# Optimization experiments

Hardware: AMD Instinct MI355X
Metric: run time of the kernel (lower is better)

Reference implementation:

```python
import jax, jax.numpy as jnp
import numpy as np

INPUT_SIZE = 32
HIDDEN = 64


def _lstm_layer(x, W_ih, W_hh, b_ih, b_hh):
    """Single LSTM layer, batch_first x: (B, T, D) -> (B, T, H).
    PyTorch gate order: i, f, g, o."""
    B, T, _ = x.shape
    H = W_hh.shape[1]
    # Precompute input contribution for all timesteps (the big GEMM).
    xg = jnp.einsum('btd,gd->btg', x, W_ih) + b_ih + b_hh  # (B, T, 4H)
    xg = jnp.swapaxes(xg, 0, 1)  # (T, B, 4H) for scan over time

    def step(carry, g_t):
        h, c = carry
        gates = g_t + h @ W_hh.T  # (B, 4H)
        i, f, g, o = jnp.split(gates, 4, axis=-1)
        c = jax.nn.sigmoid(f) * c + jax.nn.sigmoid(i) * jnp.tanh(g)
        h = jax.nn.sigmoid(o) * jnp.tanh(c)
        return (h, c), h

    h0 = jnp.zeros((B, H), dtype=x.dtype)
    c0 = jnp.zeros((B, H), dtype=x.dtype)
    (_, _), hs = jax.lax.scan(step, (h0, c0), xg)
    return jnp.swapaxes(hs, 0, 1)  # (B, T, H)


def setup_inputs() -> dict:
    key = jax.random.key(0)
    ks = jax.random.split(key, 11)
    B, T, D, H = 1024, 512, INPUT_SIZE, HIDDEN
    s_ih0 = 1.0 / np.sqrt(H)
    u = lambda k, shape: jax.random.uniform(k, shape, jnp.float32, -s_ih0, s_ih0)
    return {
        'x': jax.random.normal(ks[0], (B, T, D), jnp.float32),
        'W_ih0': u(ks[1], (4 * H, D)),
        'W_hh0': u(ks[2], (4 * H, H)),
        'b_ih0': u(ks[3], (4 * H,)),
        'b_hh0': u(ks[4], (4 * H,)),
        'W_ih1': u(ks[5], (4 * H, H)),
        'W_hh1': u(ks[6], (4 * H, H)),
        'b_ih1': u(ks[7], (4 * H,)),
        'b_hh1': u(ks[8], (4 * H,)),
        'W_fc': u(ks[9], (1, H)),
        'b_fc': u(ks[10], (1,)),
    }


def reference(x, W_ih0, W_hh0, b_ih0, b_hh0, W_ih1, W_hh1, b_ih1, b_hh1, W_fc, b_fc):
    h1 = _lstm_layer(x, W_ih0, W_hh0, b_ih0, b_hh0)   # (B, T, H)
    h2 = _lstm_layer(h1, W_ih1, W_hh1, b_ih1, b_hh1)  # (B, T, H)
    last = h2[:, -1, :]                                # (B, H)
    return last @ W_fc.T + b_fc                        # (B, 1)
```

## Files before the change

kernel.cpp:

```cpp
#include <hip/hip_runtime.h>

#define T_STEPS 512

typedef __attribute__((ext_vector_type(8))) short s16x8;
typedef __attribute__((ext_vector_type(4))) float f32x4;

__device__ __forceinline__ short f2bf(float v) {
    unsigned u = __float_as_uint(v);
    return (short)((u + 0x7FFFu + ((u >> 16) & 1u)) >> 16);
}
__device__ __forceinline__ float bf2f(short b) {
    return __uint_as_float(((unsigned)(unsigned short)b) << 16);
}
__device__ __forceinline__ float sigf(float x)  { return 1.f / (1.f + __expf(-x)); }
__device__ __forceinline__ float tanhf_(float x){ float e = __expf(2.f * x); return 1.f - 2.f / (e + 1.f); }

__global__ __launch_bounds__(1024, 4)
void lstm2_mfma(const float* __restrict__ x,
                const float* __restrict__ Wih0, const float* __restrict__ Whh0,
                const float* __restrict__ bih0, const float* __restrict__ bhh0,
                const float* __restrict__ Wih1, const float* __restrict__ Whh1,
                const float* __restrict__ bih1, const float* __restrict__ bhh1,
                const float* __restrict__ Wfc,  const float* __restrict__ bfc,
                float* __restrict__ out)
{
    __shared__ __align__(16) short vinB[2][16][104];
    __shared__ __align__(16) short u1B [2][16][136];
    __shared__ __align__(16) float gbuf0[256 * 4];
    __shared__ __align__(16) float gbuf1[256 * 4];

    const int tid  = threadIdx.x;
    const int w    = tid >> 6;
    const int lane = tid & 63;
    const int n16  = lane & 15;
    const int q4   = lane >> 4;
    const int b0   = blockIdx.x * 4;

    const int rowW = (n16 & 3) * 64 + 4 * w + (n16 >> 2);
    s16x8 a0, a1, a2;
    s16x8 e0, e1, e2, e3;
#pragma unroll
    for (int j = 0; j < 8; ++j) {
        a0[j] = f2bf(Wih0[rowW * 32 + q4 * 8 + j]);
        a1[j] = f2bf(Whh0[rowW * 64 + q4 * 8 + j]);
        a2[j] = f2bf(Whh0[rowW * 64 + 32 + q4 * 8 + j]);
        e0[j] = f2bf(Wih1[rowW * 64 + q4 * 8 + j]);
        e1[j] = f2bf(Wih1[rowW * 64 + 32 + q4 * 8 + j]);
        e2[j] = f2bf(Whh1[rowW * 64 + q4 * 8 + j]);
        e3[j] = f2bf(Whh1[rowW * 64 + 32 + q4 * 8 + j]);
    }

    const int jL = 4 * w + q4;
    f32x4 bias0, bias1;
#pragma unroll
    for (int p_ = 0; p_ < 4; ++p_) {
        bias0[p_] = bih0[p_ * 64 + jL] + bhh0[p_ * 64 + jL];
        bias1[p_] = bih1[p_ * 64 + jL] + bhh1[p_ * 64 + jL];
    }

    const int gwi = jL * 4 + n16;
    const int cw  = w & 3;
    const int cs  = 16 * cw + (lane >> 2);
    const int cb  = lane & 3;
    const int gri = 64 * cw + lane;

    const int nB  = (n16 < 4) ? n16 : 3;

    const bool isx = (w >= 8) && (w < 12) && (n16 >= 4) && (n16 < 12);
    const int  xb  = (w - 8) & 3;
    const int  xk  = q4 * 8 + ((n16 - 4) & 7);
    const float* xp = x + ((size_t)(b0 + xb) * T_STEPS) * 32 + xk;

    for (int i = tid; i < 2 * 16 * 104 / 2; i += 1024) ((int*)vinB)[i] = 0;
    for (int i = tid; i < 2 * 16 * 136 / 2; i += 1024) ((int*)u1B)[i]  = 0;
    __syncthreads();
    if (isx) vinB[0][xb][xk] = f2bf(xp[0]);
    __syncthreads();

    float cst0 = 0.f, cst1 = 0.f;

    for (int it = 0; it <= T_STEPS; ++it) {
        const int p = it & 1;

        float xpre = 0.f;
        const bool havex = isx && (it + 1 < T_STEPS);
        if (havex) xpre = xp[(size_t)(it + 1) * 32];

        const short* vb = &vinB[p][nB][q4 * 8];
        s16x8 vb0 = *(const s16x8*)(vb);
        s16x8 vb1 = *(const s16x8*)(vb + 32);
        s16x8 vb2 = *(const s16x8*)(vb + 64);
        const short* ub = &u1B[p][nB][q4 * 8];
        s16x8 ub0 = *(const s16x8*)(ub);
        s16x8 ub1 = *(const s16x8*)(ub + 32);
        s16x8 ub2 = *(const s16x8*)(ub + 64);
        s16x8 ub3 = *(const s16x8*)(ub + 96);

        f32x4 d0 = __builtin_amdgcn_mfma_f32_16x16x32_bf16(a0, vb0, bias0, 0, 0, 0);
        d0 = __builtin_amdgcn_mfma_f32_16x16x32_bf16(a1, vb1, d0, 0, 0, 0);
        d0 = __builtin_amdgcn_mfma_f32_16x16x32_bf16(a2, vb2, d0, 0, 0, 0);
        f32x4 d1 = __builtin_amdgcn_mfma_f32_16x16x32_bf16(e0, ub0, bias1, 0, 0, 0);
        d1 = __builtin_amdgcn_mfma_f32_16x16x32_bf16(e1, ub1, d1, 0, 0, 0);
        d1 = __builtin_amdgcn_mfma_f32_16x16x32_bf16(e2, ub2, d1, 0, 0, 0);
        d1 = __builtin_amdgcn_mfma_f32_16x16x32_bf16(e3, ub3, d1, 0, 0, 0);

        if (n16 < 4) {
            *(f32x4*)&gbuf0[gwi * 4] = d0;
            *(f32x4*)&gbuf1[gwi * 4] = d1;
        }
        __syncthreads();

        if (w < 4) {
            if (it < T_STEPS) {
                f32x4 g = *(const f32x4*)&gbuf0[gri * 4];
                float cc = sigf(g[1]) * cst0 + sigf(g[0]) * tanhf_(g[2]);
                cst0 = cc;
                short hb = f2bf(sigf(g[3]) * tanhf_(cc));
                vinB[p ^ 1][cb][32 + cs] = hb;
                u1B [p ^ 1][cb][cs]      = hb;
            }
        } else if (w < 8) {
            if (it >= 1) {
                f32x4 g = *(const f32x4*)&gbuf1[gri * 4];
                float cc = sigf(g[1]) * cst1 + sigf(g[0]) * tanhf_(g[2]);
                cst1 = cc;
                u1B[p ^ 1][cb][64 + cs] = f2bf(sigf(g[3]) * tanhf_(cc));
            }
        }
        if (havex) vinB[p ^ 1][xb][xk] = f2bf(xpre);
        __syncthreads();
    }

    if (tid < 4) {
        float s = bfc[0];
#pragma unroll
        for (int k = 0; k < 64; ++k)
            s += bf2f(u1B[1][tid][64 + k]) * Wfc[k];
        out[b0 + tid] = s;
    }
}

extern "C" void kernel_launch(void* const* d_in, const int* in_sizes, int n_in,
                              void* d_out, int out_size, void* d_ws, size_t ws_size,
                              hipStream_t stream) {
    const float* x    = (const float*)d_in[0];
    const float* Wih0 = (const float*)d_in[1];
    const float* Whh0 = (const float*)d_in[2];
    const float* bih0 = (const float*)d_in[3];
    const float* bhh0 = (const float*)d_in[4];
    const float* Wih1 = (const float*)d_in[5];
    const float* Whh1 = (const float*)d_in[6];
    const float* bih1 = (const float*)d_in[7];
    const float* bhh1 = (const float*)d_in[8];
    const float* Wfc  = (const float*)d_in[9];
    const float* bfc  = (const float*)d_in[10];
    float* out = (float*)d_out;

    const int B = out_size;
    dim3 grid(B / 4), block(1024);
    hipLaunchKernelGGL(lstm2_mfma, grid, block, 0, stream,
                       x, Wih0, Whh0, bih0, bhh0,
                       Wih1, Whh1, bih1, bhh1, Wfc, bfc, out);
}
```

Baseline: 584.6 us.

## Halve batch per block to 2 and give each wave two MFMA gate tiles

Each block now handles 2 batch rows with 512 threads instead of 4 rows with 1024. Each wave holds two sets of weight fragments and issues two interleaved independent MFMA chains. The goal is twice as many blocks across the GPU, cheaper block-wide barriers, and more MFMA instruction-level parallelism per wave. In exchange, only 2 of the 16 MFMA columns carry useful batch data, so more MFMA work is wasted per batch row, and register pressure rises.

```diff
diff --git a/kernel.cpp b/kernel.cpp
--- a/kernel.cpp
+++ b/kernel.cpp
@@ -15,7 +15,7 @@
 __device__ __forceinline__ float sigf(float x)  { return 1.f / (1.f + __expf(-x)); }
 __device__ __forceinline__ float tanhf_(float x){ float e = __expf(2.f * x); return 1.f - 2.f / (e + 1.f); }
 
-__global__ __launch_bounds__(1024, 4)
+__global__ __launch_bounds__(512, 4)
 void lstm2_mfma(const float* __restrict__ x,
                 const float* __restrict__ Wih0, const float* __restrict__ Whh0,
                 const float* __restrict__ bih0, const float* __restrict__ bhh0,
@@ -24,55 +24,58 @@
                 const float* __restrict__ Wfc,  const float* __restrict__ bfc,
                 float* __restrict__ out)
 {
-    __shared__ __align__(16) short vinB[2][16][104];
-    __shared__ __align__(16) short u1B [2][16][136];
-    __shared__ __align__(16) float gbuf0[256 * 4];
-    __shared__ __align__(16) float gbuf1[256 * 4];
+    __shared__ __align__(16) short vinB[2][2][104];
+    __shared__ __align__(16) short u1B [2][2][136];
+    __shared__ __align__(16) float gbuf0[128 * 4];
+    __shared__ __align__(16) float gbuf1[128 * 4];
 
     const int tid  = threadIdx.x;
     const int w    = tid >> 6;
     const int lane = tid & 63;
     const int n16  = lane & 15;
     const int q4   = lane >> 4;
-    const int b0   = blockIdx.x * 4;
+    const int b0   = blockIdx.x * 2;
 
-    const int rowW = (n16 & 3) * 64 + 4 * w + (n16 >> 2);
-    s16x8 a0, a1, a2;
-    s16x8 e0, e1, e2, e3;
+    s16x8 a0[2], a1[2], a2[2];
+    s16x8 e0[2], e1[2], e2[2], e3[2];
+    f32x4 bias0[2], bias1[2];
 #pragma unroll
-    for (int j = 0; j < 8; ++j) {
-        a0[j] = f2bf(Wih0[rowW * 32 + q4 * 8 + j]);
-        a1[j] = f2bf(Whh0[rowW * 64 + q4 * 8 + j]);
-        a2[j] = f2bf(Whh0[rowW * 64 + 32 + q4 * 8 + j]);
-        e0[j] = f2bf(Wih1[rowW * 64 + q4 * 8 + j]);
-        e1[j] = f2bf(Wih1[rowW * 64 + 32 + q4 * 8 + j]);
-        e2[j] = f2bf(Whh1[rowW * 64 + q4 * 8 + j]);
-        e3[j] = f2bf(Whh1[rowW * 64 + 32 + q4 * 8 + j]);
+    for (int t = 0; t < 2; ++t) {
+        const int rowW = (n16 & 3) * 64 + 8 * w + 4 * t + (n16 >> 2);
+#pragma unroll
+        for (int j = 0; j < 8; ++j) {
+            a0[t][j] = f2bf(Wih0[rowW * 32 + q4 * 8 + j]);
+            a1[t][j] = f2bf(Whh0[rowW * 64 + q4 * 8 + j]);
+            a2[t][j] = f2bf(Whh0[rowW * 64 + 32 + q4 * 8 + j]);
+            e0[t][j] = f2bf(Wih1[rowW * 64 + q4 * 8 + j]);
+            e1[t][j] = f2bf(Wih1[rowW * 64 + 32 + q4 * 8 + j]);
+            e2[t][j] = f2bf(Whh1[rowW * 64 + q4 * 8 + j]);
+            e3[t][j] = f2bf(Whh1[rowW * 64 + 32 + q4 * 8 + j]);
+        }
+        const int jl = 8 * w + 4 * t + q4;
+#pragma unroll
+        for (int p_ = 0; p_ < 4; ++p_) {
+            bias0[t][p_] = bih0[p_ * 64 + jl] + bhh0[p_ * 64 + jl];
+            bias1[t][p_] = bih1[p_ * 64 + jl] + bhh1[p_ * 64 + jl];
+        }
     }
 
-    const int jL = 4 * w + q4;
-    f32x4 bias0, bias1;
-#pragma unroll
-    for (int p_ = 0; p_ < 4; ++p_) {
-        bias0[p_] = bih0[p_ * 64 + jL] + bhh0[p_ * 64 + jL];
-        bias1[p_] = bih1[p_ * 64 + jL] + bhh1[p_ * 64 + jL];
-    }
+    const int gw0 = ((8 * w + q4) * 2 + n16) * 4;
+    const int gw1 = ((8 * w + 4 + q4) * 2 + n16) * 4;
+    const int cw2 = w & 1;
+    const int cs  = 32 * cw2 + (lane >> 1);
+    const int cb  = lane & 1;
+    const int gri = 64 * cw2 + lane;
 
-    const int gwi = jL * 4 + n16;
-    const int cw  = w & 3;
-    const int cs  = 16 * cw + (lane >> 2);
-    const int cb  = lane & 3;
-    const int gri = 64 * cw + lane;
+    const int nB  = (n16 < 2) ? n16 : 1;
 
-    const int nB  = (n16 < 4) ? n16 : 3;
-
-    const bool isx = (w >= 8) && (w < 12) && (n16 >= 4) && (n16 < 12);
-    const int  xb  = (w - 8) & 3;
-    const int  xk  = q4 * 8 + ((n16 - 4) & 7);
+    const bool isx = (w == 4);
+    const int  xb  = lane >> 5;
+    const int  xk  = lane & 31;
     const float* xp = x + ((size_t)(b0 + xb) * T_STEPS) * 32 + xk;
 
-    for (int i = tid; i < 2 * 16 * 104 / 2; i += 1024) ((int*)vinB)[i] = 0;
-    for (int i = tid; i < 2 * 16 * 136 / 2; i += 1024) ((int*)u1B)[i]  = 0;
+    for (int i = tid; i < 2 * 2 * 104 / 2; i += 512) ((int*)vinB)[i] = 0;
+    for (int i = tid; i < 2 * 2 * 136 / 2; i += 512) ((int*)u1B)[i]  = 0;
     __syncthreads();
     if (isx) vinB[0][xb][xk] = f2bf(xp[0]);
     __syncthreads();
@@ -90,27 +93,38 @@
         s16x8 vb0 = *(const s16x8*)(vb);
         s16x8 vb1 = *(const s16x8*)(vb + 32);
         s16x8 vb2 = *(const s16x8*)(vb + 64);
+
+        f32x4 d0a = __builtin_amdgcn_mfma_f32_16x16x32_bf16(a0[0], vb0, bias0[0], 0, 0, 0);
+        f32x4 d0b = __builtin_amdgcn_mfma_f32_16x16x32_bf16(a0[1], vb0, bias0[1], 0, 0, 0);
+        d0a = __builtin_amdgcn_mfma_f32_16x16x32_bf16(a1[0], vb1, d0a, 0, 0, 0);
+        d0b = __builtin_amdgcn_mfma_f32_16x16x32_bf16(a1[1], vb1, d0b, 0, 0, 0);
+        d0a = __builtin_amdgcn_mfma_f32_16x16x32_bf16(a2[0], vb2, d0a, 0, 0, 0);
+        d0b = __builtin_amdgcn_mfma_f32_16x16x32_bf16(a2[1], vb2, d0b, 0, 0, 0);
+
         const short* ub = &u1B[p][nB][q4 * 8];
         s16x8 ub0 = *(const s16x8*)(ub);
         s16x8 ub1 = *(const s16x8*)(ub + 32);
         s16x8 ub2 = *(const s16x8*)(ub + 64);
         s16x8 ub3 = *(const s16x8*)(ub + 96);
 
-        f32x4 d0 = __builtin_amdgcn_mfma_f32_16x16x32_bf16(a0, vb0, bias0, 0, 0, 0);
-        d0 = __builtin_amdgcn_mfma_f32_16x16x32_bf16(a1, vb1, d0, 0, 0, 0);
-        d0 = __builtin_amdgcn_mfma_f32_16x16x32_bf16(a2, vb2, d0, 0, 0, 0);
-        f32x4 d1 = __builtin_amdgcn_mfma_f32_16x16x32_bf16(e0, ub0, bias1, 0, 0, 0);
-        d1 = __builtin_amdgcn_mfma_f32_16x16x32_bf16(e1, ub1, d1, 0, 0, 0);
-        d1 = __builtin_amdgcn_mfma_f32_16x16x32_bf16(e2, ub2, d1, 0, 0, 0);
-        d1 = __builtin_amdgcn_mfma_f32_16x16x32_bf16(e3, ub3, d1, 0, 0, 0);
+        f32x4 d1a = __builtin_amdgcn_mfma_f32_16x16x32_bf16(e0[0], ub0, bias1[0], 0, 0, 0);
+        f32x4 d1b = __builtin_amdgcn_mfma_f32_16x16x32_bf16(e0[1], ub0, bias1[1], 0, 0, 0);
+        d1a = __builtin_amdgcn_mfma_f32_16x16x32_bf16(e1[0], ub1, d1a, 0, 0, 0);
+        d1b = __builtin_amdgcn_mfma_f32_16x16x32_bf16(e1[1], ub1, d1b, 0, 0, 0);
+        d1a = __builtin_amdgcn_mfma_f32_16x16x32_bf16(e2[0], ub2, d1a, 0, 0, 0);
+        d1b = __builtin_amdgcn_mfma_f32_16x16x32_bf16(e2[1], ub2, d1b, 0, 0, 0);
+        d1a = __builtin_amdgcn_mfma_f32_16x16x32_bf16(e3[0], ub3, d1a, 0, 0, 0);
+        d1b = __builtin_amdgcn_mfma_f32_16x16x32_bf16(e3[1], ub3, d1b, 0, 0, 0);
 
-        if (n16 < 4) {
-            *(f32x4*)&gbuf0[gwi * 4] = d0;
-            *(f32x4*)&gbuf1[gwi * 4] = d1;
+        if (n16 < 2) {
+            *(f32x4*)&gbuf0[gw0] = d0a;
+            *(f32x4*)&gbuf0[gw1] = d0b;
+            *(f32x4*)&gbuf1[gw0] = d1a;
+            *(f32x4*)&gbuf1[gw1] = d1b;
         }
         __syncthreads();
 
-        if (w < 4) {
+        if (w < 2) {
             if (it < T_STEPS) {
                 f32x4 g = *(const f32x4*)&gbuf0[gri * 4];
                 float cc = sigf(g[1]) * cst0 + sigf(g[0]) * tanhf_(g[2]);
@@ -119,7 +133,7 @@
                 vinB[p ^ 1][cb][32 + cs] = hb;
                 u1B [p ^ 1][cb][cs]      = hb;
             }
-        } else if (w < 8) {
+        } else if (w < 4) {
             if (it >= 1) {
                 f32x4 g = *(const f32x4*)&gbuf1[gri * 4];
                 float cc = sigf(g[1]) * cst1 + sigf(g[0]) * tanhf_(g[2]);
@@ -131,7 +145,7 @@
         __syncthreads();
     }
 
-    if (tid < 4) {
+    if (tid < 2) {
         float s = bfc[0];
 #pragma unroll
         for (int k = 0; k < 64; ++k)
@@ -157,7 +171,7 @@
     float* out = (float*)d_out;
 
     const int B = out_size;
-    dim3 grid(B / 4), block(1024);
+    dim3 grid(B / 2), block(512);
     hipLaunchKernelGGL(lstm2_mfma, grid, block, 0, stream,
                        x, Wih0, Whh0, bih0, bhh0,
                        Wih1, Whh1, bih1, bhh1, Wfc, bfc, out);
```

Result: slower. 653.4 us (+11.8%).

## Merge LSTM layer input buffers into one shared LDS buffer and use fast exp/rcp

Applied to the files above, without the earlier changes.

Merges the two per-layer B-operand LDS buffers into one contiguous buffer [x | h1 | h2], so the layer-1 h value is written once and shared by both MFMA chains. This drops one LDS store per step and two B-fragment loads per step. The sigmoid and tanh helpers now call the hardware exp2 and rcp builtins instead of expf and division, and the launch bounds become an explicit waves-per-eu attribute. The single cell-state register works because each wave handles only one layer. The approximate reciprocal adds a small precision loss.

```diff
diff --git a/kernel.cpp b/kernel.cpp
--- a/kernel.cpp
+++ b/kernel.cpp
@@ -12,10 +12,13 @@
 __device__ __forceinline__ float bf2f(short b) {
     return __uint_as_float(((unsigned)(unsigned short)b) << 16);
 }
-__device__ __forceinline__ float sigf(float x)  { return 1.f / (1.f + __expf(-x)); }
-__device__ __forceinline__ float tanhf_(float x){ float e = __expf(2.f * x); return 1.f - 2.f / (e + 1.f); }
+#define LOG2E 1.4426950408889634f
+__device__ __forceinline__ float rcpf(float x)  { return __builtin_amdgcn_rcpf(x); }
+__device__ __forceinline__ float ex2f(float x)  { return __builtin_amdgcn_exp2f(x); }
+__device__ __forceinline__ float sigf(float x)  { return rcpf(1.f + ex2f(-LOG2E * x)); }
+__device__ __forceinline__ float tanhf_(float x){ return 1.f - 2.f * rcpf(ex2f(2.f * LOG2E * x) + 1.f); }
 
-__global__ __launch_bounds__(1024, 4)
+__global__ __launch_bounds__(1024) __attribute__((amdgpu_waves_per_eu(4, 4)))
 void lstm2_mfma(const float* __restrict__ x,
                 const float* __restrict__ Wih0, const float* __restrict__ Whh0,
                 const float* __restrict__ bih0, const float* __restrict__ bhh0,
@@ -24,8 +27,7 @@
                 const float* __restrict__ Wfc,  const float* __restrict__ bfc,
                 float* __restrict__ out)
 {
-    __shared__ __align__(16) short vinB[2][16][104];
-    __shared__ __align__(16) short u1B [2][16][136];
+    __shared__ __align__(16) short bB[2][4][176];
     __shared__ __align__(16) float gbuf0[256 * 4];
     __shared__ __align__(16) float gbuf1[256 * 4];
 
@@ -58,7 +60,7 @@
         bias1[p_] = bih1[p_ * 64 + jL] + bhh1[p_ * 64 + jL];
     }
 
-    const int gwi = jL * 4 + n16;
+    const int gwi = (jL * 4 + n16) * 4;
     const int cw  = w & 3;
     const int cs  = 16 * cw + (lane >> 2);
     const int cb  = lane & 3;
@@ -71,13 +73,12 @@
     const int  xk  = q4 * 8 + ((n16 - 4) & 7);
     const float* xp = x + ((size_t)(b0 + xb) * T_STEPS) * 32 + xk;
 
-    for (int i = tid; i < 2 * 16 * 104 / 2; i += 1024) ((int*)vinB)[i] = 0;
-    for (int i = tid; i < 2 * 16 * 136 / 2; i += 1024) ((int*)u1B)[i]  = 0;
+    for (int i = tid; i < 2 * 4 * 176 / 2; i += 1024) ((int*)bB)[i] = 0;
     __syncthreads();
-    if (isx) vinB[0][xb][xk] = f2bf(xp[0]);
+    if (isx) bB[0][xb][xk] = f2bf(xp[0]);
     __syncthreads();
 
-    float cst0 = 0.f, cst1 = 0.f;
+    float cst = 0.f;
 
     for (int it = 0; it <= T_STEPS; ++it) {
         const int p = it & 1;
@@ -86,48 +87,43 @@
         const bool havex = isx && (it + 1 < T_STEPS);
         if (havex) xpre = xp[(size_t)(it + 1) * 32];
 
-        const short* vb = &vinB[p][nB][q4 * 8];
-        s16x8 vb0 = *(const s16x8*)(vb);
-        s16x8 vb1 = *(const s16x8*)(vb + 32);
-        s16x8 vb2 = *(const s16x8*)(vb + 64);
-        const short* ub = &u1B[p][nB][q4 * 8];
-        s16x8 ub0 = *(const s16x8*)(ub);
-        s16x8 ub1 = *(const s16x8*)(ub + 32);
-        s16x8 ub2 = *(const s16x8*)(ub + 64);
-        s16x8 ub3 = *(const s16x8*)(ub + 96);
+        const short* bp = &bB[p][nB][q4 * 8];
+        s16x8 t0 = *(const s16x8*)(bp);
+        s16x8 t1 = *(const s16x8*)(bp + 32);
+        s16x8 t2 = *(const s16x8*)(bp + 64);
+        s16x8 t3 = *(const s16x8*)(bp + 96);
+        s16x8 t4 = *(const s16x8*)(bp + 128);
 
-        f32x4 d0 = __builtin_amdgcn_mfma_f32_16x16x32_bf16(a0, vb0, bias0, 0, 0, 0);
-        d0 = __builtin_amdgcn_mfma_f32_16x16x32_bf16(a1, vb1, d0, 0, 0, 0);
-        d0 = __builtin_amdgcn_mfma_f32_16x16x32_bf16(a2, vb2, d0, 0, 0, 0);
-        f32x4 d1 = __builtin_amdgcn_mfma_f32_16x16x32_bf16(e0, ub0, bias1, 0, 0, 0);
-        d1 = __builtin_amdgcn_mfma_f32_16x16x32_bf16(e1, ub1, d1, 0, 0, 0);
-        d1 = __builtin_amdgcn_mfma_f32_16x16x32_bf16(e2, ub2, d1, 0, 0, 0);
-        d1 = __builtin_amdgcn_mfma_f32_16x16x32_bf16(e3, ub3, d1, 0, 0, 0);
+        f32x4 d0 = __builtin_amdgcn_mfma_f32_16x16x32_bf16(a0, t0, bias0, 0, 0, 0);
+        d0 = __builtin_amdgcn_mfma_f32_16x16x32_bf16(a1, t1, d0, 0, 0, 0);
+        d0 = __builtin_amdgcn_mfma_f32_16x16x32_bf16(a2, t2, d0, 0, 0, 0);
+        f32x4 d1 = __builtin_amdgcn_mfma_f32_16x16x32_bf16(e0, t1, bias1, 0, 0, 0);
+        d1 = __builtin_amdgcn_mfma_f32_16x16x32_bf16(e1, t2, d1, 0, 0, 0);
+        d1 = __builtin_amdgcn_mfma_f32_16x16x32_bf16(e2, t3, d1, 0, 0, 0);
+        d1 = __builtin_amdgcn_mfma_f32_16x16x32_bf16(e3, t4, d1, 0, 0, 0);
 
         if (n16 < 4) {
-            *(f32x4*)&gbuf0[gwi * 4] = d0;
-            *(f32x4*)&gbuf1[gwi * 4] = d1;
+            *(f32x4*)&gbuf0[gwi] = d0;
+            *(f32x4*)&gbuf1[gwi] = d1;
         }
         __syncthreads();
 
         if (w < 4) {
             if (it < T_STEPS) {
                 f32x4 g = *(const f32x4*)&gbuf0[gri * 4];
-                float cc = sigf(g[1]) * cst0 + sigf(g[0]) * tanhf_(g[2]);
-                cst0 = cc;
-                short hb = f2bf(sigf(g[3]) * tanhf_(cc));
-                vinB[p ^ 1][cb][32 + cs] = hb;
-                u1B [p ^ 1][cb][cs]      = hb;
+                float cc = sigf(g[1]) * cst + sigf(g[0]) * tanhf_(g[2]);
+                cst = cc;
+                bB[p ^ 1][cb][32 + cs] = f2bf(sigf(g[3]) * tanhf_(cc));
             }
         } else if (w < 8) {
             if (it >= 1) {
                 f32x4 g = *(const f32x4*)&gbuf1[gri * 4];
-                float cc = sigf(g[1]) * cst1 + sigf(g[0]) * tanhf_(g[2]);
-                cst1 = cc;
-                u1B[p ^ 1][cb][64 + cs] = f2bf(sigf(g[3]) * tanhf_(cc));
+                float cc = sigf(g[1]) * cst + sigf(g[0]) * tanhf_(g[2]);
+                cst = cc;
+                bB[p ^ 1][cb][96 + cs] = f2bf(sigf(g[3]) * tanhf_(cc));
             }
         }
-        if (havex) vinB[p ^ 1][xb][xk] = f2bf(xpre);
+        if (havex) bB[p ^ 1][xb][xk] = f2bf(xpre);
         __syncthreads();
     }
 
@@ -135,7 +131,7 @@
         float s = bfc[0];
 #pragma unroll
         for (int k = 0; k < 64; ++k)
-            s += bf2f(u1B[1][tid][64 + k]) * Wfc[k];
+            s += bf2f(bB[1][tid][96 + k]) * Wfc[k];
         out[b0 + tid] = s;
     }
 }
```

Result: faster. 479.8 us (-17.9%).
